# Optimization experiments

Measured on AMD Instinct MI355X. Metric: run time of the kernel, lower is better.

The kernel has to match this reference:

```python
import jax, jax.numpy as jnp
import numpy as np

B, C, D, H, W = 4, 256, 16, 16, 16


def setup_inputs() -> dict:
    key = jax.random.key(0)
    ks = jax.random.split(key, 9)
    s = 1.0 / np.sqrt(C)
    inp = {
        "x": jax.random.normal(ks[0], (B, C, D, H, W), dtype=jnp.float32),
        "wq": jax.random.normal(ks[1], (C, C), dtype=jnp.float32) * s,
        "bq": jax.random.normal(ks[2], (C,), dtype=jnp.float32) * 0.02,
        "wk": jax.random.normal(ks[3], (C, C), dtype=jnp.float32) * s,
        "bk": jax.random.normal(ks[4], (C,), dtype=jnp.float32) * 0.02,
        "wv": jax.random.normal(ks[5], (C, C), dtype=jnp.float32) * s,
        "bv": jax.random.normal(ks[6], (C,), dtype=jnp.float32) * 0.02,
        "wp": jax.random.normal(ks[7], (C, C), dtype=jnp.float32) * s,
        "bp": jax.random.normal(ks[8], (C,), dtype=jnp.float32) * 0.02,
    }
    return inp


def reference(x, wq, bq, wk, bk, wv, bv, wp, bp):
    b, c, d, h, w = x.shape
    xf = x.reshape(b, c, d * h * w)  # (B, C, N)
    # 1x1 Conv3d == per-voxel linear map over channels
    q = jnp.einsum('oc,bcn->bon', wq, xf) + bq[:, None]
    k = jnp.einsum('oc,bcn->bon', wk, xf) + bk[:, None]
    v = jnp.einsum('oc,bcn->bon', wv, xf) + bv[:, None]
    # scores[b,i,j] = q[:, :, i] . k[:, :, j], scaled AFTER the bmm (as in source)
    scores = jnp.einsum('bci,bcj->bij', q, k) * (c ** -0.5)
    p = jax.nn.softmax(scores, axis=2)  # (B, N, N), softmax over keys j
    # attention[b,c,i] = sum_j v[b,c,j] * p[b,i,j]
    attn = jnp.einsum('bcj,bij->bci', v, p)
    out = jnp.einsum('oc,bcn->bon', wp, attn) + bp[:, None]
    return x + out.reshape(b, c, d, h, w)
```

## Files before the change

kernel.cpp:

```cpp
#include <hip/hip_runtime.h>

typedef unsigned short u16;
typedef unsigned int u32;
typedef __bf16 v8bf __attribute__((ext_vector_type(8)));
typedef float v4f __attribute__((ext_vector_type(4)));

#define DEV __device__ __forceinline__

constexpr int CB = 4;
constexpr int C = 256;
constexpr int NN = 4096;
constexpr float LOG2E = 1.4426950408889634f;
constexpr int PST = 44;

DEV u16 f2bf(float f) {
  union { float f; u32 u; } v; v.f = f;
  u32 r = v.u + 0x7fffu + ((v.u >> 16) & 1u);
  return (u16)(r >> 16);
}
DEV float bf2f(u16 h) {
  union { u32 u; float f; } v; v.u = ((u32)h) << 16; return v.f;
}

DEV void dma16(const u16* g, const u16* lds_base) {
  __builtin_amdgcn_global_load_lds(
      (const __attribute__((address_space(1))) void*)(unsigned long long)g,
      (__attribute__((address_space(3))) void*)(u32)(unsigned long long)lds_base,
      16, 0, 0);
}

__global__ __launch_bounds__(256) void k_transpose(const float* __restrict__ x,
                                                   u16* __restrict__ xT) {
  __shared__ float tile[32][33];
  int b = blockIdx.z;
  int n0 = blockIdx.x * 32, c0 = blockIdx.y * 32;
  int tx = threadIdx.x & 31, ty = threadIdx.x >> 5;
  const float* xb = x + (long)b * C * NN;
#pragma unroll
  for (int r = 0; r < 4; ++r)
    tile[ty + r * 8][tx] = xb[(long)(c0 + ty + r * 8) * NN + n0 + tx];
  __syncthreads();
  u16* xTb = xT + (long)b * NN * C;
#pragma unroll
  for (int r = 0; r < 4; ++r)
    xTb[(long)(n0 + ty + r * 8) * C + c0 + tx] = f2bf(tile[tx][ty + r * 8]);
}

__global__ __launch_bounds__(256) void k_cvt4(const float* __restrict__ s0,
                                              const float* __restrict__ s1,
                                              const float* __restrict__ s2,
                                              const float* __restrict__ s3,
                                              u16* __restrict__ d0, u16* __restrict__ d1,
                                              u16* __restrict__ d2, u16* __restrict__ d3,
                                              float* __restrict__ Mbuf) {
  if (blockIdx.x == 0 && blockIdx.y == 0 && threadIdx.x < 8) Mbuf[threadIdx.x] = 0.f;
  int wsel = blockIdx.y;
  const float* s = wsel == 0 ? s0 : wsel == 1 ? s1 : wsel == 2 ? s2 : s3;
  u16* d = wsel == 0 ? d0 : wsel == 1 ? d1 : wsel == 2 ? d2 : d3;
  int i = blockIdx.x * 256 + threadIdx.x;
  d[i] = f2bf(s[i]);
}

DEV void stage_dma(const u16* __restrict__ g, const u16* lds, int w, int lane) {
#pragma unroll
  for (int i = 0; i < 8; ++i) {
    int idx = w * 8 + i;
    int r = idx * 2 + (lane >> 5);
    int cg = (lane & 31) ^ (r & 7);
    dma16(g + (long)r * 256 + cg * 8, lds + idx * 512);
  }
}

__global__ __launch_bounds__(256) void k_qkv(
    const u16* __restrict__ xT, const u16* __restrict__ wqb, const u16* __restrict__ wkb,
    const u16* __restrict__ wvb, const float* __restrict__ bq, const float* __restrict__ bk,
    const float* __restrict__ bv, u16* __restrict__ qO, u16* __restrict__ kO,
    u16* __restrict__ vO) {
  __shared__ __align__(16) u16 Ash[64 * 256];
  __shared__ __align__(16) u16 Bsh[64 * 256];
  int t = threadIdx.x, w = t >> 6, lane = t & 63, lr = lane & 15, q = lane >> 4;
  int m0 = blockIdx.x * 64, n0 = blockIdx.y * 64, b = blockIdx.z;
  const int xk = lr & 7;
  stage_dma(xT + (long)b * NN * C + (long)m0 * 256, Ash, w, lane);
  stage_dma(wqb + (long)n0 * 256, Bsh, w, lane);
  asm volatile("s_waitcnt vmcnt(0)\n\ts_barrier" ::: "memory");
#pragma unroll 1
  for (int wsel = 0; wsel < 3; ++wsel) {
    v4f acc[4];
#pragma unroll
    for (int nt = 0; nt < 4; ++nt)
#pragma unroll
      for (int r = 0; r < 4; ++r) acc[nt][r] = 0.f;
#pragma unroll
    for (int ks = 0; ks < 8; ++ks) {
      int cg = ((ks * 4 + q) ^ xk) << 3;
      v8bf a = *reinterpret_cast<const v8bf*>(Ash + (w * 16 + lr) * 256 + cg);
#pragma unroll
      for (int nt = 0; nt < 4; ++nt) {
        v8bf bb = *reinterpret_cast<const v8bf*>(Bsh + (nt * 16 + lr) * 256 + cg);
        acc[nt] = __builtin_amdgcn_mfma_f32_16x16x32_bf16(a, bb, acc[nt], 0, 0, 0);
      }
    }
    asm volatile("s_waitcnt lgkmcnt(0)\n\ts_barrier" ::: "memory");
    if (wsel < 2) {
      stage_dma((wsel == 0 ? wkb : wvb) + (long)n0 * 256, Bsh, w, lane);
      const float* bias = wsel == 0 ? bq : bk;
#pragma unroll
      for (int nt = 0; nt < 4; ++nt) {
#pragma unroll
        for (int r = 0; r < 4; ++r) {
          int gm = m0 + w * 16 + q * 4 + r;
          int gn = n0 + nt * 16 + lr;
          float val = acc[nt][r] + bias[gn];
          if (wsel == 0) {
            qO[((long)b * NN + gm) * C + gn] = f2bf(val * (0.0625f * LOG2E));
          } else {
            kO[((long)b * NN + gm) * C + gn] = f2bf(val);
          }
        }
      }
      asm volatile("s_waitcnt vmcnt(0)\n\ts_barrier" ::: "memory");
    } else {
      u16* Vt = Ash;
#pragma unroll
      for (int nt = 0; nt < 4; ++nt) {
#pragma unroll
        for (int r = 0; r < 4; ++r) {
          int gn_l = nt * 16 + lr;
          int gm_l = w * 16 + q * 4 + r;
          float val = acc[nt][r] + bv[n0 + gn_l];
          Vt[gn_l * 72 + gm_l] = f2bf(val);
        }
      }
      asm volatile("s_waitcnt lgkmcnt(0)\n\ts_barrier" ::: "memory");
      int row = t >> 2;
      u16* vrow = vO + (long)b * C * NN + (long)(n0 + row) * NN + m0;
#pragma unroll
      for (int s2 = 0; s2 < 2; ++s2) {
        int seg = (t & 3) * 2 + s2;
        *reinterpret_cast<uint4*>(vrow + seg * 8) =
            *reinterpret_cast<const uint4*>(Vt + row * 72 + seg * 8);
      }
    }
  }
}

__global__ __launch_bounds__(256) void k_maxnorm(const u16* __restrict__ qT,
                                                 const u16* __restrict__ kT,
                                                 float* __restrict__ Mbuf) {
  int b = blockIdx.z, tsel = blockIdx.y;
  const u16* src = (tsel ? kT : qT) + (long)b * NN * C;
  int row = blockIdx.x * 64 + (threadIdx.x >> 2);
  const uint4* pp =
      reinterpret_cast<const uint4*>(src + (long)row * C + (threadIdx.x & 3) * 64);
  float s = 0.f;
#pragma unroll
  for (int u = 0; u < 8; ++u) {
    uint4 d = pp[u];
    const u16* e = reinterpret_cast<const u16*>(&d);
#pragma unroll
    for (int i = 0; i < 8; ++i) { float f = bf2f(e[i]); s += f * f; }
  }
  s += __shfl_xor(s, 1, 64);
  s += __shfl_xor(s, 2, 64);
#pragma unroll
  for (int d2 = 4; d2 < 64; d2 <<= 1) s = fmaxf(s, __shfl_xor(s, d2, 64));
  if ((threadIdx.x & 63) == 0)
    atomicMax((u32*)(Mbuf + tsel * 4 + b), __float_as_uint(s));
}

__global__ __launch_bounds__(256) void k_gemm(
    const u16* __restrict__ A, long aStr, const u16* __restrict__ Bm, long bStr,
    const float* __restrict__ biasM, const float* __restrict__ biasN,
    const float* __restrict__ resid, long rStr, float scale,
    float* __restrict__ outF, u16* __restrict__ outH, long oStr, int ldm, int ldn) {
  __shared__ __align__(16) u16 Ash[64 * 256];
  __shared__ __align__(16) u16 Bsh[64 * 256];
  int t = threadIdx.x;
  int w = t >> 6, lane = t & 63, lr = lane & 15, q = lane >> 4;
  int m0 = blockIdx.x * 64, n0 = blockIdx.y * 64, b = blockIdx.z;
  const int xk = lr & 7;
  stage_dma(A + b * aStr + (long)m0 * 256, Ash, w, lane);
  stage_dma(Bm + b * bStr + (long)n0 * 256, Bsh, w, lane);
  asm volatile("s_waitcnt vmcnt(0)\n\ts_barrier" ::: "memory");
  v4f acc[4];
#pragma unroll
  for (int nt = 0; nt < 4; ++nt)
#pragma unroll
    for (int r = 0; r < 4; ++r) acc[nt][r] = 0.f;
#pragma unroll
  for (int ks = 0; ks < 8; ++ks) {
    int cg = ((ks * 4 + q) ^ xk) << 3;
    v8bf a = *reinterpret_cast<const v8bf*>(Ash + (w * 16 + lr) * 256 + cg);
#pragma unroll
    for (int nt = 0; nt < 4; ++nt) {
      v8bf bb = *reinterpret_cast<const v8bf*>(Bsh + (nt * 16 + lr) * 256 + cg);
      acc[nt] = __builtin_amdgcn_mfma_f32_16x16x32_bf16(a, bb, acc[nt], 0, 0, 0);
    }
  }
#pragma unroll
  for (int nt = 0; nt < 4; ++nt) {
#pragma unroll
    for (int r = 0; r < 4; ++r) {
      int gm = m0 + w * 16 + q * 4 + r;
      int gn = n0 + nt * 16 + lr;
      float val = acc[nt][r];
      if (biasM) val += biasM[gm];
      if (biasN) val += biasN[gn];
      val *= scale;
      long addr = b * oStr + (long)gm * ldm + (long)gn * ldn;
      if (resid) val += resid[b * rStr + (long)gm * ldm + (long)gn * ldn];
      if (outF) outF[addr] = val;
      else outH[addr] = f2bf(val);
    }
  }
}

DEV void kissue(const u16* kb, const u16* kshb, int j0, int w, int lane) {
#pragma unroll
  for (int i = 0; i < 4; ++i) {
    int idx = w * 4 + i;
    int kr = idx * 2 + (lane >> 5);
    int kc = (lane & 31) ^ (kr & 7);
    dma16(kb + (long)(j0 + kr) * 256 + kc * 8, kshb + idx * 512);
  }
}

#define FLASH_STEP(IT, VL, VU, PW, PR, KC, KN)                                     \
  {                                                                                \
    int jn_ = ((IT) + 1 < niter) ? jstart + (((IT) + 1) << 5) : jstart;            \
    kissue(kb, (KN), jn_, w, lane);                                                \
    asm volatile("" ::: "memory");    \
    {                                                                              \
      int jv_ = jstart + ((IT) << 5);                                              \
      _Pragma("unroll") for (int cs = 0; cs < 4; ++cs)                             \
          VL[cs] = *reinterpret_cast<const v8bf*>(                                 \
              vbw + (long)(cs * 16 + lr) * NN + jv_ + q * 8);                      \
    }                                                                              \
    v4f s0_, s1_;                                                                  \
    _Pragma("unroll") for (int r = 0; r < 4; ++r) { s0_[r] = 0.f; s1_[r] = 0.f; }  \
    _Pragma("unroll") for (int ks = 0; ks < 8; ++ks) {                             \
      int cg_ = ((ks * 4 + q) ^ xk) << 3;                                          \
      v8bf k0_ = *reinterpret_cast<const v8bf*>((KC) + lr * 256 + cg_);            \
      v8bf k1_ = *reinterpret_cast<const v8bf*>((KC) + (16 + lr) * 256 + cg_);     \
      s0_ = __builtin_amdgcn_mfma_f32_16x16x32_bf16(qf[ks], k0_, s0_, 0, 0, 0);    \
      s1_ = __builtin_amdgcn_mfma_f32_16x16x32_bf16(qf[ks], k1_, s1_, 0, 0, 0);    \
    }                                                                              \
    _Pragma("unroll") for (int r = 0; r < 4; ++r) {                                \
      float p0_ = exp2f(s0_[r] - M);                                               \
      float p1_ = exp2f(s1_[r] - M);                                               \
      lsum[r] += p0_ + p1_;                                                        \
      (PW)[(q * 4 + r) * PST + lr] = (u16)((__float_as_uint(p0_) + 0x8000u) >> 16);\
      (PW)[(q * 4 + r) * PST + 16 + lr] =                                          \
          (u16)((__float_as_uint(p1_) + 0x8000u) >> 16);                           \
    }                                                                              \
    if ((IT) > 0) {                                                                \
      v8bf pa_[4];                                                                 \
      _Pragma("unroll") for (int qs = 0; qs < 4; ++qs)                             \
          pa_[qs] = *reinterpret_cast<const v8bf*>(                                \
              (PR) + (qs * 16 + lr) * PST + q * 8);                                \
      _Pragma("unroll") for (int cs = 0; cs < 4; ++cs)                             \
        _Pragma("unroll") for (int qs = 0; qs < 4; ++qs)                           \
          accO[qs * 4 + cs] = __builtin_amdgcn_mfma_f32_16x16x32_bf16(             \
              pa_[qs], VU[cs], accO[qs * 4 + cs], 0, 0, 0);                        \
    }                                                                              \
    asm volatile("s_waitcnt vmcnt(4) lgkmcnt(0)\n\ts_barrier" ::: "memory");       \
  }

__global__ __launch_bounds__(256, 2) void k_flash(const u16* __restrict__ qT,
                                                  const u16* __restrict__ kT,
                                                  const u16* __restrict__ V,
                                                  u16* __restrict__ op0,
                                                  u16* __restrict__ op1,
                                                  u16* __restrict__ op2,
                                                  u16* __restrict__ op3,
                                                  float* __restrict__ ml,
                                                  const float* __restrict__ Mbuf,
                                                  int span) {
  __shared__ __align__(16) u16 ksh[2][32 * 256];
  __shared__ __align__(16) u16 psh[2][64 * PST];
  int t = threadIdx.x;
  int w = t >> 6, lane = t & 63, lr = lane & 15, q = lane >> 4;
  int b = blockIdx.z, h = blockIdx.y;
  int i0 = blockIdx.x * 64;
  const u16* qb = qT + ((long)b * NN + i0 + w * 16) * C;
  const u16* kb = kT + (long)b * NN * C;
  const u16* vbw = V + (long)b * C * NN + (long)(w * 64) * NN;
  float M = sqrtf(Mbuf[b] * Mbuf[4 + b]) + 1.0f;

  v8bf qf[8];
#pragma unroll
  for (int ks = 0; ks < 8; ++ks)
    qf[ks] = *reinterpret_cast<const v8bf*>(qb + lr * C + ks * 32 + q * 8);

  v4f accO[16];
#pragma unroll
  for (int ct = 0; ct < 16; ++ct)
#pragma unroll
    for (int r = 0; r < 4; ++r) accO[ct][r] = 0.f;
  float lsum[4] = {0.f, 0.f, 0.f, 0.f};

  u16* pw0 = psh[0] + w * 16 * PST;
  u16* pw1 = psh[1] + w * 16 * PST;
  const int xk = lr & 7;

  int jstart = h * span;
  int niter = span >> 5;

  kissue(kb, ksh[0], jstart, w, lane);
  asm volatile("s_waitcnt vmcnt(0)\n\ts_barrier" ::: "memory");

  v8bf vA[4] = {}, vB[4] = {};
#pragma unroll 1
  for (int it2 = 0; it2 < niter; it2 += 2) {
    FLASH_STEP(it2,     vA, vB, pw0, psh[1], ksh[0], ksh[1])
    FLASH_STEP(it2 + 1, vB, vA, pw1, psh[0], ksh[1], ksh[0])
  }
  {
    v8bf pa_[4];
#pragma unroll
    for (int qs = 0; qs < 4; ++qs)
      pa_[qs] = *reinterpret_cast<const v8bf*>(psh[1] + (qs * 16 + lr) * PST + q * 8);
#pragma unroll
    for (int cs = 0; cs < 4; ++cs)
#pragma unroll
      for (int qs = 0; qs < 4; ++qs)
        accO[qs * 4 + cs] = __builtin_amdgcn_mfma_f32_16x16x32_bf16(
            pa_[qs], vB[cs], accO[qs * 4 + cs], 0, 0, 0);
  }

#pragma unroll
  for (int r = 0; r < 4; ++r) {
#pragma unroll
    for (int d = 1; d < 16; d <<= 1) lsum[r] += __shfl_xor(lsum[r], d, 64);
  }
  u16* opp = h == 0 ? op0 : h == 1 ? op1 : h == 2 ? op2 : op3;
  u16* ob = opp + ((long)b * NN + i0) * C;
#pragma unroll
  for (int qs = 0; qs < 4; ++qs)
#pragma unroll
    for (int cs = 0; cs < 4; ++cs)
#pragma unroll
      for (int r = 0; r < 4; ++r)
        ob[(qs * 16 + q * 4 + r) * C + w * 64 + cs * 16 + lr] =
            f2bf(accO[qs * 4 + cs][r]);
  if (lr == 0) {
    long rbase = ((long)h * CB + b) * NN + i0 + w * 16 + q * 4;
#pragma unroll
    for (int r = 0; r < 4; ++r) {
      ml[(rbase + r) * 2] = M;
      ml[(rbase + r) * 2 + 1] = lsum[r];
    }
  }
}

__global__ __launch_bounds__(256) void k_combine(const u16* __restrict__ p0,
                                                 const u16* __restrict__ p1,
                                                 const u16* __restrict__ p2,
                                                 const u16* __restrict__ p3,
                                                 const float* __restrict__ ml,
                                                 u16* __restrict__ o, int js) {
  long row = (long)blockIdx.x * 8 + (threadIdx.x >> 5);
  int tc = (threadIdx.x & 31) * 8;
  float m[4], l[4];
  float mx = -3.0e38f;
  for (int h = 0; h < js; ++h) {
    m[h] = ml[((long)h * CB * NN + row) * 2];
    l[h] = ml[((long)h * CB * NN + row) * 2 + 1];
    mx = fmaxf(mx, m[h]);
  }
  float tot = 0.f, a[4];
  for (int h = 0; h < js; ++h) { a[h] = exp2f(m[h] - mx); tot += a[h] * l[h]; }
  float inv = 1.f / tot;
  float acc[8];
#pragma unroll
  for (int i = 0; i < 8; ++i) acc[i] = 0.f;
  const u16* ps[4] = {p0, p1, p2, p3};
  for (int h = 0; h < js; ++h) {
    uint4 u = *reinterpret_cast<const uint4*>(ps[h] + row * C + tc);
    const u16* p = reinterpret_cast<const u16*>(&u);
    float wgt = a[h] * inv;
#pragma unroll
    for (int i = 0; i < 8; ++i) acc[i] += wgt * bf2f(p[i]);
  }
  u16 outv[8];
#pragma unroll
  for (int i = 0; i < 8; ++i) outv[i] = f2bf(acc[i]);
  *reinterpret_cast<uint4*>(o + row * C + tc) = *reinterpret_cast<const uint4*>(outv);
}

extern "C" void kernel_launch(void* const* d_in, const int* in_sizes, int n_in,
                              void* d_out, int out_size, void* d_ws, size_t ws_size,
                              hipStream_t stream) {
  const float* x = (const float*)d_in[0];
  const float* wq = (const float*)d_in[1];
  const float* bq = (const float*)d_in[2];
  const float* wk = (const float*)d_in[3];
  const float* bk = (const float*)d_in[4];
  const float* wv = (const float*)d_in[5];
  const float* bv = (const float*)d_in[6];
  const float* wp = (const float*)d_in[7];
  const float* bp = (const float*)d_in[8];
  float* out = (float*)d_out;
  char* ws = (char*)d_ws;

  const long SLOT = 8388608L;
  const size_t NEED4 = 524288UL + 7 * 8388608UL + 524288UL + 4096UL;
  int js = (ws_size >= NEED4) ? 4 : 2;

  u16* wqb = (u16*)(ws + 0);
  u16* wkb = (u16*)(ws + 131072L);
  u16* wvb = (u16*)(ws + 262144L);
  u16* wpb = (u16*)(ws + 393216L);
  char* base = ws + 524288L;
  u16* xT  = (u16*)(base);
  u16* qTw = (u16*)(base + 1 * SLOT);
  u16* kTw = (u16*)(base + 2 * SLOT);
  u16* vw  = (u16*)(base + 3 * SLOT);
  u16* op1 = (u16*)(base + 4 * SLOT);
  u16* op2 = js == 4 ? (u16*)(base + 5 * SLOT) : op1;
  u16* op3 = js == 4 ? (u16*)(base + 6 * SLOT) : op1;
  float* ml = (float*)(base + (js == 4 ? 7 : 5) * SLOT);
  float* Mbuf = ml + 131072;
  u16* op0 = xT;
  u16* oW  = qTw;

  k_cvt4<<<dim3(256, 4), 256, 0, stream>>>(wq, wk, wv, wp, wqb, wkb, wvb, wpb, Mbuf);
  k_transpose<<<dim3(128, 8, CB), 256, 0, stream>>>(x, xT);
  k_qkv<<<dim3(64, 4, CB), 256, 0, stream>>>(xT, wqb, wkb, wvb, bq, bk, bv, qTw, kTw, vw);
  k_maxnorm<<<dim3(64, 2, CB), 256, 0, stream>>>(qTw, kTw, Mbuf);
  k_flash<<<dim3(64, js, CB), 256, 0, stream>>>(qTw, kTw, vw, op0, op1, op2, op3, ml,
                                                Mbuf, NN / js);
  k_combine<<<2048, 256, 0, stream>>>(op0, op1, op2, op3, ml, oW, js);

  long nc = (long)NN * C;
  k_gemm<<<dim3(4, 64, CB), 256, 0, stream>>>(wpb, 0, oW, nc, bp, nullptr, x, nc,
                                              1.0f, out, nullptr, nc, NN, 1);
}
```

Before: 267.9 us.

## Fuse row-norm partials into QKV epilogue and remap flash block order

The QKV projection epilogue now accumulates per-row squared norms of the scaled Q and of K from fp32 values and writes partial sums per column-tile into a scratch buffer. A tiny k_norm kernel then reduces those partials into the max norm, replacing the separate pass that re-read the whole bf16 Q and K tensors. The flash kernel also remaps its flat block index so that consecutive blocks are spread across batches and heads, presumably to balance work or cache use across XCDs. The softmax bound margin changes from 1.0 to 1.5 to allow for the norms now being computed from fp32 instead of rounded bf16 values.

```diff
diff --git a/kernel.cpp b/kernel.cpp
--- a/kernel.cpp
+++ b/kernel.cpp
@@ -75,7 +75,7 @@
     const u16* __restrict__ xT, const u16* __restrict__ wqb, const u16* __restrict__ wkb,
     const u16* __restrict__ wvb, const float* __restrict__ bq, const float* __restrict__ bk,
     const float* __restrict__ bv, u16* __restrict__ qO, u16* __restrict__ kO,
-    u16* __restrict__ vO) {
+    u16* __restrict__ vO, float* __restrict__ Pn) {
   __shared__ __align__(16) u16 Ash[64 * 256];
   __shared__ __align__(16) u16 Bsh[64 * 256];
   int t = threadIdx.x, w = t >> 6, lane = t & 63, lr = lane & 15, q = lane >> 4;
@@ -105,6 +105,7 @@
     if (wsel < 2) {
       stage_dma((wsel == 0 ? wkb : wvb) + (long)n0 * 256, Bsh, w, lane);
       const float* bias = wsel == 0 ? bq : bk;
+      float sn[4] = {0.f, 0.f, 0.f, 0.f};
 #pragma unroll
       for (int nt = 0; nt < 4; ++nt) {
 #pragma unroll
@@ -113,11 +114,25 @@
           int gn = n0 + nt * 16 + lr;
           float val = acc[nt][r] + bias[gn];
           if (wsel == 0) {
-            qO[((long)b * NN + gm) * C + gn] = f2bf(val * (0.0625f * LOG2E));
+            float vs = val * (0.0625f * LOG2E);
+            qO[((long)b * NN + gm) * C + gn] = f2bf(vs);
+            sn[r] += vs * vs;
           } else {
             kO[((long)b * NN + gm) * C + gn] = f2bf(val);
+            sn[r] += val * val;
           }
         }
+      }
+#pragma unroll
+      for (int r = 0; r < 4; ++r) {
+#pragma unroll
+        for (int d = 1; d < 16; d <<= 1) sn[r] += __shfl_xor(sn[r], d, 64);
+      }
+      if (lr == 0) {
+#pragma unroll
+        for (int r = 0; r < 4; ++r)
+          Pn[(((long)wsel * 4 + blockIdx.y) * CB + b) * NN + m0 + w * 16 + q * 4 + r] =
+              sn[r];
       }
       asm volatile("s_waitcnt vmcnt(0)\n\ts_barrier" ::: "memory");
     } else {
@@ -145,28 +160,21 @@
   }
 }
 
-__global__ __launch_bounds__(256) void k_maxnorm(const u16* __restrict__ qT,
-                                                 const u16* __restrict__ kT,
-                                                 float* __restrict__ Mbuf) {
-  int b = blockIdx.z, tsel = blockIdx.y;
-  const u16* src = (tsel ? kT : qT) + (long)b * NN * C;
-  int row = blockIdx.x * 64 + (threadIdx.x >> 2);
-  const uint4* pp =
-      reinterpret_cast<const uint4*>(src + (long)row * C + (threadIdx.x & 3) * 64);
-  float s = 0.f;
-#pragma unroll
-  for (int u = 0; u < 8; ++u) {
-    uint4 d = pp[u];
-    const u16* e = reinterpret_cast<const u16*>(&d);
-#pragma unroll
-    for (int i = 0; i < 8; ++i) { float f = bf2f(e[i]); s += f * f; }
-  }
-  s += __shfl_xor(s, 1, 64);
-  s += __shfl_xor(s, 2, 64);
-#pragma unroll
-  for (int d2 = 4; d2 < 64; d2 <<= 1) s = fmaxf(s, __shfl_xor(s, d2, 64));
+__global__ __launch_bounds__(256) void k_norm(const float* __restrict__ Pn,
+                                              float* __restrict__ Mbuf) {
+  int tsel = blockIdx.y, b = blockIdx.z;
+  float mx = 0.f;
+  for (int row = threadIdx.x; row < NN; row += 256) {
+    float s = 0.f;
+#pragma unroll
+    for (int qr = 0; qr < 4; ++qr)
+      s += Pn[(((long)tsel * 4 + qr) * CB + b) * NN + row];
+    mx = fmaxf(mx, s);
+  }
+#pragma unroll
+  for (int d = 1; d < 64; d <<= 1) mx = fmaxf(mx, __shfl_xor(mx, d, 64));
   if ((threadIdx.x & 63) == 0)
-    atomicMax((u32*)(Mbuf + tsel * 4 + b), __float_as_uint(s));
+    atomicMax((u32*)(Mbuf + tsel * 4 + b), __float_as_uint(mx));
 }
 
 __global__ __launch_bounds__(256) void k_gemm(
@@ -281,12 +289,16 @@
   __shared__ __align__(16) u16 psh[2][64 * PST];
   int t = threadIdx.x;
   int w = t >> 6, lane = t & 63, lr = lane & 15, q = lane >> 4;
-  int b = blockIdx.z, h = blockIdx.y;
-  int i0 = blockIdx.x * 64;
+  int total = gridDim.x * gridDim.y * gridDim.z;
+  int flat = blockIdx.x + gridDim.x * (blockIdx.y + gridDim.y * blockIdx.z);
+  int nf = (flat & 7) * (total >> 3) + (flat >> 3);
+  int h = (nf >> 6) & (gridDim.y - 1);
+  int b = nf >> (6 + __builtin_ctz(gridDim.y));
+  int i0 = (nf & 63) * 64;
   const u16* qb = qT + ((long)b * NN + i0 + w * 16) * C;
   const u16* kb = kT + (long)b * NN * C;
   const u16* vbw = V + (long)b * C * NN + (long)(w * 64) * NN;
-  float M = sqrtf(Mbuf[b] * Mbuf[4 + b]) + 1.0f;
+  float M = sqrtf(Mbuf[b] * Mbuf[4 + b]) + 1.5f;
 
   v8bf qf[8];
 #pragma unroll
@@ -424,11 +436,13 @@
   float* Mbuf = ml + 131072;
   u16* op0 = xT;
   u16* oW  = qTw;
+  float* Pn = (float*)op1;
 
   k_cvt4<<<dim3(256, 4), 256, 0, stream>>>(wq, wk, wv, wp, wqb, wkb, wvb, wpb, Mbuf);
   k_transpose<<<dim3(128, 8, CB), 256, 0, stream>>>(x, xT);
-  k_qkv<<<dim3(64, 4, CB), 256, 0, stream>>>(xT, wqb, wkb, wvb, bq, bk, bv, qTw, kTw, vw);
-  k_maxnorm<<<dim3(64, 2, CB), 256, 0, stream>>>(qTw, kTw, Mbuf);
+  k_qkv<<<dim3(64, 4, CB), 256, 0, stream>>>(xT, wqb, wkb, wvb, bq, bk, bv, qTw, kTw,
+                                             vw, Pn);
+  k_norm<<<dim3(1, 2, CB), 256, 0, stream>>>(Pn, Mbuf);
   k_flash<<<dim3(64, js, CB), 256, 0, stream>>>(qTw, kTw, vw, op0, op1, op2, op3, ml,
                                                 Mbuf, NN / js);
   k_combine<<<2048, 256, 0, stream>>>(op0, op1, op2, op3, ml, oW, js);
```

Measured after the change: 246.0 us. 8.2% less time.
